# Performance work log

Hardware: AMD Instinct MI355X
Metric: run time of the kernel (lower is better)

The kernel has to match this reference:

```python
import jax, jax.numpy as jnp
import numpy as np

NUM_HEADS = 8
EMBED_DIM = 512
MAX_SEQ = 2048
HEAD_DIM = EMBED_DIM // NUM_HEADS
B, S = 2, 2048


def setup_inputs() -> dict:
    key = jax.random.key(0)
    ks = jax.random.split(key, 12)
    sd = 1.0 / np.sqrt(EMBED_DIM)
    return {
        "q_in": jax.random.normal(ks[0], (B, S, EMBED_DIM), jnp.float32),
        "k_in": jax.random.normal(ks[1], (B, S, EMBED_DIM), jnp.float32),
        "v_in": jax.random.normal(ks[2], (B, S, EMBED_DIM), jnp.float32),
        "Wq": jax.random.normal(ks[3], (EMBED_DIM, EMBED_DIM), jnp.float32) * sd,
        "bq": jnp.zeros((EMBED_DIM,), jnp.float32),
        "Wk": jax.random.normal(ks[4], (EMBED_DIM, EMBED_DIM), jnp.float32) * sd,
        "bk": jnp.zeros((EMBED_DIM,), jnp.float32),
        "Wv": jax.random.normal(ks[5], (EMBED_DIM, EMBED_DIM), jnp.float32) * sd,
        "bv": jnp.zeros((EMBED_DIM,), jnp.float32),
        "Wo": jax.random.normal(ks[6], (EMBED_DIM, EMBED_DIM), jnp.float32) * sd,
        "bo": jnp.zeros((EMBED_DIM,), jnp.float32),
        "rel_emb": jax.random.normal(ks[7], (MAX_SEQ, HEAD_DIM), jnp.float32) * sd,
    }


def _split_heads(x, W, b):
    # x: [B,S,E] -> [B,H,S,D]
    y = x @ W + b
    b_, s_ = y.shape[0], y.shape[1]
    return y.reshape(b_, s_, NUM_HEADS, HEAD_DIM).transpose(0, 2, 1, 3)


def _relative_scores(q, rel_emb):
    # q: [B,H,L,D]; rel_emb sliced to last L rows: [M,D] with M == L here
    L = q.shape[2]
    rel = rel_emb[max(0, MAX_SEQ - L):, :]
    M = rel.shape[0]
    scores = jnp.einsum('bhld,md->bhlm', q, rel)
    # mask = flip(tri(L,M), axis=-1): zero out future relative positions
    mask = jnp.flip(jnp.tri(L, M, dtype=jnp.float32), axis=1)
    scores = scores * mask
    # skew trick: pad one column on the left, reshape swapping last two dims, drop first row
    padded = jnp.pad(scores, ((0, 0), (0, 0), (0, 0), (1, 0)))  # [B,H,L,M+1]
    reshaped = padded.reshape(padded.shape[0], padded.shape[1], M + 1, L)
    skewed = reshaped[:, :, 1:, :]  # [B,H,M,L] == [B,H,L,L]
    return skewed


def reference(q_in, k_in, v_in, Wq, bq, Wk, bk, Wv, bv, Wo, bo, rel_emb):
    q = _split_heads(q_in, Wq, bq)  # [B,H,S,D]
    k = _split_heads(k_in, Wk, bk)
    v = _split_heads(v_in, Wv, bv)
    scores = jnp.einsum('bhqd,bhkd->bhqk', q, k)
    rel_scores = _relative_scores(q, rel_emb)
    logits = (scores + rel_scores) / jnp.sqrt(jnp.float32(HEAD_DIM))
    attn = jax.nn.softmax(logits, axis=-1)
    out = jnp.einsum('bhqk,bhkd->bhqd', attn, v)  # [B,H,S,D]
    merged = out.transpose(0, 2, 1, 3).reshape(out.shape[0], -1, EMBED_DIM)
    return merged @ Wo + bo, attn
```

## Files before the change

kernel.cpp:

```cpp
#include <hip/hip_runtime.h>


typedef __attribute__((ext_vector_type(4))) float f32x4;
typedef __attribute__((ext_vector_type(8))) short short8;

__device__ inline unsigned short f2bf(float x) {
    unsigned u = __float_as_uint(x);
    unsigned r = (u + 0x7fffu + ((u >> 16) & 1u)) >> 16;
    return (unsigned short)r;
}
__device__ inline float bf2f(unsigned short h) {
    return __uint_as_float(((unsigned)h) << 16);
}
__device__ inline int swz(int row, int bytecol) {
    return (row << 7) + (bytecol ^ ((row & 7) << 4));
}
__device__ inline void cvt4(float4 v, uint2& hi, uint2& lo) {
    unsigned short h0 = f2bf(v.x), h1 = f2bf(v.y), h2 = f2bf(v.z), h3 = f2bf(v.w);
    hi = make_uint2(((unsigned)h1 << 16) | h0, ((unsigned)h3 << 16) | h2);
    lo = make_uint2(((unsigned)f2bf(v.y - bf2f(h1)) << 16) | f2bf(v.x - bf2f(h0)),
                    ((unsigned)f2bf(v.w - bf2f(h3)) << 16) | f2bf(v.z - bf2f(h2)));
}

__global__ __launch_bounds__(256) void wt_prep4(const float* __restrict__ W0,
                                                const float* __restrict__ W1,
                                                const float* __restrict__ W2,
                                                const float* __restrict__ W3,
                                                unsigned short* __restrict__ wt)
{
    __shared__ float Ls[32][33];
    const int t = threadIdx.x;
    const int z = blockIdx.z;
    const float* W = (z == 0) ? W0 : (z == 1) ? W1 : (z == 2) ? W2 : W3;
    unsigned short* WTh = wt + (size_t)(2 * z) * 262144;
    unsigned short* WTl = wt + (size_t)(2 * z + 1) * 262144;
    const int k0 = blockIdx.x << 5, n0 = blockIdx.y << 5;
#pragma unroll
    for (int i = 0; i < 4; ++i) {
        int idx = (i << 8) + t;
        int kk = idx >> 5, nn = idx & 31;
        Ls[kk][nn] = W[(size_t)(k0 + kk) * 512 + n0 + nn];
    }
    __syncthreads();
#pragma unroll
    for (int i = 0; i < 2; ++i) {
        int idx = (i << 8) + t;
        int nn = idx >> 4, kp = idx & 15;
        float f0 = Ls[2 * kp][nn], f1 = Ls[2 * kp + 1][nn];
        unsigned short h0 = f2bf(f0), h1 = f2bf(f1);
        size_t off = (size_t)(n0 + nn) * 512 + k0 + 2 * kp;
        *(unsigned*)&WTh[off] = ((unsigned)h1 << 16) | h0;
        *(unsigned*)&WTl[off] = ((unsigned)f2bf(f1 - bf2f(h1)) << 16) | f2bf(f0 - bf2f(h0));
    }
}

__global__ __launch_bounds__(256) void rel_prep(const float* __restrict__ rel,
                                                unsigned short* __restrict__ relh)
{
    int idx = (blockIdx.x * 256 + threadIdx.x) << 3;
    float4 a = *(const float4*)&rel[idx];
    float4 b = *(const float4*)&rel[idx + 4];
    uint4 o;
    o.x = ((unsigned)f2bf(a.y) << 16) | f2bf(a.x);
    o.y = ((unsigned)f2bf(a.w) << 16) | f2bf(a.z);
    o.z = ((unsigned)f2bf(b.y) << 16) | f2bf(b.x);
    o.w = ((unsigned)f2bf(b.w) << 16) | f2bf(b.z);
    *(uint4*)&relh[idx] = o;
}

__device__ __forceinline__ void gemm64_core(const float* __restrict__ A,
                                            const unsigned short* __restrict__ WTh,
                                            const unsigned short* __restrict__ WTl,
                                            int m0, int n0, char* smem, int t,
                                            f32x4 (&acc)[4])
{
    char* aH = smem;
    char* aL = smem + 8192;
    char* wH = smem + 16384;
    char* wL = smem + 24576;
    const int lane = t & 63, w = t >> 6;
    const int lr = lane & 15, kg = lane >> 4;

    for (int k0 = 0; k0 < 512; k0 += 64) {
        if (k0) __syncthreads();
#pragma unroll
        for (int i = 0; i < 4; ++i) {
            int idx = (i << 8) + t;
            int row = idx >> 4, c4 = idx & 15;
            float4 v = *(const float4*)&A[(size_t)(m0 + row) * 512 + k0 + (c4 << 2)];
            uint2 hi, lo; cvt4(v, hi, lo);
            int ph = swz(row, c4 << 3);
            *(uint2*)(aH + ph) = hi;
            *(uint2*)(aL + ph) = lo;
        }
#pragma unroll
        for (int i = 0; i < 4; ++i) {
            int idx = (i << 8) + t;
            int plane = idx >> 9, rem = idx & 511;
            int nn = rem >> 3, j8 = rem & 7;
            const unsigned short* src = plane ? WTl : WTh;
            uint4 vv = *(const uint4*)&src[(size_t)(n0 + nn) * 512 + k0 + (j8 << 3)];
            *(uint4*)((plane ? wL : wH) + swz(nn, j8 << 4)) = vv;
        }
        __syncthreads();
#pragma unroll
        for (int kk = 0; kk < 2; ++kk) {
            int bc = (kk << 6) + (kg << 4);
            int ar = (w << 4) + lr;
            short8 a_h = *(const short8*)(aH + swz(ar, bc));
            short8 a_l = *(const short8*)(aL + swz(ar, bc));
#pragma unroll
            for (int f = 0; f < 4; ++f) {
                short8 b_h = *(const short8*)(wH + swz((f << 4) + lr, bc));
                short8 b_l = *(const short8*)(wL + swz((f << 4) + lr, bc));
                acc[f] = __builtin_amdgcn_mfma_f32_16x16x32_bf16(a_h, b_h, acc[f], 0, 0, 0);
                acc[f] = __builtin_amdgcn_mfma_f32_16x16x32_bf16(a_l, b_h, acc[f], 0, 0, 0);
                acc[f] = __builtin_amdgcn_mfma_f32_16x16x32_bf16(a_h, b_l, acc[f], 0, 0, 0);
            }
        }
    }
}

__global__ __launch_bounds__(256) void gemm_qkv(
    const float* __restrict__ Aq, const float* __restrict__ Ak, const float* __restrict__ Av,
    const unsigned short* __restrict__ wt,
    const float* __restrict__ bq, const float* __restrict__ bk, const float* __restrict__ bv,
    unsigned short* __restrict__ qh, unsigned short* __restrict__ ql,
    unsigned short* __restrict__ kh, unsigned short* __restrict__ kl,
    unsigned short* __restrict__ vh, unsigned short* __restrict__ vl)
{
    __shared__ char smem[32768];
    const int t = threadIdx.x;
    const int z = blockIdx.z;
    const int n0 = blockIdx.x << 6;
    const int m0 = blockIdx.y << 6;
    const int lane = t & 63, w = t >> 6;
    const int lr = lane & 15, kg = lane >> 4;

    const float* A = (z == 0) ? Aq : (z == 1) ? Ak : Av;
    const float* bias = (z == 0) ? bq : (z == 1) ? bk : bv;
    const unsigned short* WTh = wt + (size_t)(2 * z) * 262144;
    const unsigned short* WTl = wt + (size_t)(2 * z + 1) * 262144;
    unsigned short* outH = (z == 0) ? qh : (z == 1) ? kh : vh;
    unsigned short* outL = (z == 0) ? ql : (z == 1) ? kl : vl;

    f32x4 acc[4];
#pragma unroll
    for (int f = 0; f < 4; ++f) acc[f] = {0.f, 0.f, 0.f, 0.f};

    gemm64_core(A, WTh, WTl, m0, n0, smem, t, acc);

    const int mbase = m0 + (w << 4) + (kg << 2);
    const int b = mbase >> 11, s = mbase & 2047;
    const int bidx = (b << 3) + (n0 >> 6);
#pragma unroll
    for (int f = 0; f < 4; ++f) {
        int d = (f << 4) + lr;
        float bv_ = bias[n0 + d];
        if (z < 2) {
#pragma unroll
            for (int e = 0; e < 4; ++e) {
                float val = acc[f][e] + bv_;
                unsigned short hh = f2bf(val);
                size_t off = ((size_t)bidx * 2048 + s + e) * 64 + d;
                outH[off] = hh;
                outL[off] = f2bf(val - bf2f(hh));
            }
        } else {
            unsigned short h[4], l[4];
#pragma unroll
            for (int e = 0; e < 4; ++e) {
                float val = acc[f][e] + bv_;
                h[e] = f2bf(val);
                l[e] = f2bf(val - bf2f(h[e]));
            }
            size_t off = ((size_t)bidx * 64 + d) * 2048 + s;
            *(uint2*)&outH[off] = make_uint2(((unsigned)h[1] << 16) | h[0],
                                             ((unsigned)h[3] << 16) | h[2]);
            *(uint2*)&outL[off] = make_uint2(((unsigned)l[1] << 16) | l[0],
                                             ((unsigned)l[3] << 16) | l[2]);
        }
    }
}

__global__ __launch_bounds__(256) void gemm_out(
    const unsigned short* __restrict__ mWh, const unsigned short* __restrict__ mWl,
    const unsigned short* __restrict__ WTh, const unsigned short* __restrict__ WTl,
    const float* __restrict__ bias, float* __restrict__ out0)
{
    __shared__ char smem[32768];
    char* aH = smem;
    char* aL = smem + 8192;
    char* wH = smem + 16384;
    char* wL = smem + 24576;
    const int t = threadIdx.x;
    const int n0 = blockIdx.x << 6;
    const int m0 = blockIdx.y << 6;
    const int lane = t & 63, w = t >> 6;
    const int lr = lane & 15, kg = lane >> 4;

    f32x4 acc[4];
#pragma unroll
    for (int f = 0; f < 4; ++f) acc[f] = {0.f, 0.f, 0.f, 0.f};

    for (int k0 = 0; k0 < 512; k0 += 64) {
        if (k0) __syncthreads();
#pragma unroll
        for (int i = 0; i < 4; ++i) {
            int idx = (i << 8) + t;
            int plane = idx >> 9, rem = idx & 511;
            int row = rem >> 3, j8 = rem & 7;
            const unsigned short* src = plane ? mWl : mWh;
            uint4 vv = *(const uint4*)&src[(size_t)(m0 + row) * 512 + k0 + (j8 << 3)];
            *(uint4*)((plane ? aL : aH) + swz(row, j8 << 4)) = vv;
        }
#pragma unroll
        for (int i = 0; i < 4; ++i) {
            int idx = (i << 8) + t;
            int plane = idx >> 9, rem = idx & 511;
            int nn = rem >> 3, j8 = rem & 7;
            const unsigned short* src = plane ? WTl : WTh;
            uint4 vv = *(const uint4*)&src[(size_t)(n0 + nn) * 512 + k0 + (j8 << 3)];
            *(uint4*)((plane ? wL : wH) + swz(nn, j8 << 4)) = vv;
        }
        __syncthreads();
#pragma unroll
        for (int kk = 0; kk < 2; ++kk) {
            int bc = (kk << 6) + (kg << 4);
            int ar = (w << 4) + lr;
            short8 a_h = *(const short8*)(aH + swz(ar, bc));
            short8 a_l = *(const short8*)(aL + swz(ar, bc));
#pragma unroll
            for (int f = 0; f < 4; ++f) {
                short8 b_h = *(const short8*)(wH + swz((f << 4) + lr, bc));
                short8 b_l = *(const short8*)(wL + swz((f << 4) + lr, bc));
                acc[f] = __builtin_amdgcn_mfma_f32_16x16x32_bf16(a_h, b_h, acc[f], 0, 0, 0);
                acc[f] = __builtin_amdgcn_mfma_f32_16x16x32_bf16(a_l, b_h, acc[f], 0, 0, 0);
                acc[f] = __builtin_amdgcn_mfma_f32_16x16x32_bf16(a_h, b_l, acc[f], 0, 0, 0);
            }
        }
    }

    const int mbase = m0 + (w << 4) + (kg << 2);
#pragma unroll
    for (int f = 0; f < 4; ++f) {
        int n = n0 + (f << 4) + lr;
        float bv = bias[n];
#pragma unroll
        for (int e = 0; e < 4; ++e)
            out0[(size_t)(mbase + e) * 512 + n] = acc[f][e] + bv;
    }
}

__global__ __launch_bounds__(512, 4) void logits_flash(
    const unsigned short* __restrict__ qh_g, const unsigned short* __restrict__ ql_g,
    const unsigned short* __restrict__ kh_g, const unsigned short* __restrict__ kl_g,
    const unsigned short* __restrict__ relh_g,
    float* __restrict__ attn, float2* __restrict__ stats)
{
    __shared__ char smem[59136];
    char* kh = smem;
    char* kl = smem + 16384;
    char* bandP = smem + 32768;
    unsigned short* Pt = (unsigned short*)(smem + 32768);
    float* part_m = (float*)(smem + 58112);
    float* part_z = (float*)(smem + 58624);

    const int t = threadIdx.x;
    const int bh = blockIdx.y;
    int ib = blockIdx.x; if (bh & 8) ib = 31 - ib;
    const int i0 = ib << 6;
    const int lane = t & 63, w = t >> 6;
    const int wr = w >> 1, wc = w & 1;
    const int lr = lane & 15, kg = lane >> 4;
    const int irow = (wr << 4) + lr;

    const size_t qoff = ((size_t)bh * 2048 + i0 + irow) * 64;
    const short8 aH0 = *(const short8*)(qh_g + qoff + (kg << 3));
    const short8 aH1 = *(const short8*)(qh_g + qoff + 32 + (kg << 3));
    const short8 aL0 = *(const short8*)(ql_g + qoff + (kg << 3));
    const short8 aL1 = *(const short8*)(ql_g + qoff + 32 + (kg << 3));

    float rm = -3.0e38f, rz = 0.f;

    const unsigned short* khb = kh_g + (size_t)bh * 2048 * 64;
    const unsigned short* klb = kl_g + (size_t)bh * 2048 * 64;
    const size_t obase = ((size_t)bh * 2048 + i0) * 2048;

    for (int jt = 0; jt < 16; ++jt) {
        const int j0 = jt << 7;
        const bool anyRel = (j0 <= i0 + 63);
        const int m0 = 1984 - i0 + j0;
        __syncthreads();
        {
            int rr = t >> 2, gp = (t & 3) << 1;
            const unsigned short* s0 = khb + (size_t)(j0 + rr) * 64 + (gp << 3);
            *(uint4*)(kh + swz(rr, gp << 4)) = *(const uint4*)s0;
            *(uint4*)(kh + swz(rr, (gp + 1) << 4)) = *(const uint4*)(s0 + 8);
            const unsigned short* s1 = klb + (size_t)(j0 + rr) * 64 + (gp << 3);
            *(uint4*)(kl + swz(rr, gp << 4)) = *(const uint4*)s1;
            *(uint4*)(kl + swz(rr, (gp + 1) << 4)) = *(const uint4*)(s1 + 8);
        }
        if (anyRel) {
#pragma unroll
            for (int i = 0; i < 3; ++i) {
                int idx = (i << 9) + t;
                int row = idx >> 3, g = idx & 7;
                int m = m0 + row; if (m > 2047) m = 2047;
                *(uint4*)(bandP + swz(row, g << 4)) = *(const uint4*)(relh_g + (size_t)m * 64 + (g << 3));
            }
        }
        __syncthreads();

        f32x4 acc[4];
#pragma unroll
        for (int cf = 0; cf < 4; ++cf) {
            int krow = (wc << 6) + (cf << 4) + lr;
            short8 bH0 = *(const short8*)(kh + swz(krow, kg << 4));
            short8 bH1 = *(const short8*)(kh + swz(krow, 64 + (kg << 4)));
            short8 bL0 = *(const short8*)(kl + swz(krow, kg << 4));
            short8 bL1 = *(const short8*)(kl + swz(krow, 64 + (kg << 4)));
            f32x4 c = {0.f, 0.f, 0.f, 0.f};
            c = __builtin_amdgcn_mfma_f32_16x16x32_bf16(bH0, aH0, c, 0, 0, 0);
            c = __builtin_amdgcn_mfma_f32_16x16x32_bf16(bH1, aH1, c, 0, 0, 0);
            c = __builtin_amdgcn_mfma_f32_16x16x32_bf16(bH0, aL0, c, 0, 0, 0);
            c = __builtin_amdgcn_mfma_f32_16x16x32_bf16(bH1, aL1, c, 0, 0, 0);
            c = __builtin_amdgcn_mfma_f32_16x16x32_bf16(bL0, aH0, c, 0, 0, 0);
            c = __builtin_amdgcn_mfma_f32_16x16x32_bf16(bL1, aH1, c, 0, 0, 0);
            acc[cf] = c;
        }
        if (anyRel) {
            f32x4 pr[6];
#pragma unroll
            for (int q = 0; q < 6; ++q) {
                int ff = (wc ? 6 : 0) + q;
                int brow = (ff << 4) + lr;
                short8 rb0 = *(const short8*)(bandP + swz(brow, kg << 4));
                short8 rb1 = *(const short8*)(bandP + swz(brow, 64 + (kg << 4)));
                f32x4 c = {0.f, 0.f, 0.f, 0.f};
                c = __builtin_amdgcn_mfma_f32_16x16x32_bf16(rb0, aH0, c, 0, 0, 0);
                c = __builtin_amdgcn_mfma_f32_16x16x32_bf16(rb1, aH1, c, 0, 0, 0);
                pr[q] = c;
            }
            __syncthreads();
#pragma unroll
            for (int q = 0; q < 6; ++q) {
                int ff = (wc ? 6 : 0) + q;
#pragma unroll
                for (int e = 0; e < 4; ++e)
                    Pt[((ff << 4) + (kg << 2) + e) * 66 + irow] = f2bf(pr[q][e]);
            }
            __syncthreads();
        }

        float rowmax = -3.0e38f;
#pragma unroll
        for (int cf = 0; cf < 4; ++cf) {
            int jl0 = (wc << 6) + (cf << 4) + (kg << 2);
            f32x4 a = acc[cf];
#pragma unroll
            for (int e = 0; e < 4; ++e) {
                int jl = jl0 + e;
                if (anyRel && (jl - irow) <= (i0 - j0))
                    a[e] += bf2f(Pt[(jl + 63 - irow) * 66 + irow]);
            }
            acc[cf] = a;
            *(float4*)&attn[obase + (size_t)irow * 2048 + j0 + jl0] =
                make_float4(a[0], a[1], a[2], a[3]);
            rowmax = fmaxf(rowmax, fmaxf(fmaxf(a[0], a[1]), fmaxf(a[2], a[3])));
        }
        rowmax = fmaxf(rowmax, __shfl_xor(rowmax, 16, 64));
        rowmax = fmaxf(rowmax, __shfl_xor(rowmax, 32, 64));
        float zs = 0.f;
#pragma unroll
        for (int cf = 0; cf < 4; ++cf)
#pragma unroll
            for (int e = 0; e < 4; ++e)
                zs += __expf((acc[cf][e] - rowmax) * 0.125f);
        zs += __shfl_xor(zs, 16, 64);
        zs += __shfl_xor(zs, 32, 64);
        if (lane < 16) {
            part_m[(wc << 6) + irow] = rowmax;
            part_z[(wc << 6) + irow] = zs;
        }
        __syncthreads();
        if (t < 64) {
            float m1 = part_m[t], m2 = part_m[64 + t];
            float z1 = part_z[t], z2 = part_z[64 + t];
            float tm = fmaxf(m1, m2);
            float tz = z1 * __expf((m1 - tm) * 0.125f) + z2 * __expf((m2 - tm) * 0.125f);
            float mn = fmaxf(rm, tm);
            rz = rz * __expf((rm - mn) * 0.125f) + tz * __expf((tm - mn) * 0.125f);
            rm = mn;
        }
    }
    if (t < 64) stats[bh * 2048 + i0 + t] = make_float2(rm, 1.0f / rz);
}

__global__ __launch_bounds__(256) void pv_fused(float* __restrict__ attn,
                                                const unsigned short* __restrict__ vTh,
                                                const unsigned short* __restrict__ vTl,
                                                const float2* __restrict__ stats,
                                                float* __restrict__ pO)
{
    __shared__ char smem[33280];
    char* pH = smem;
    char* pL = smem + 8192;
    char* vH = smem + 16384;
    char* vL = smem + 24576;
    float2* sm = (float2*)(smem + 32768);

    const int t = threadIdx.x;
    const int i0 = blockIdx.x << 6;
    const int bh = blockIdx.y;
    const int jc = blockIdx.z;
    const int jc0 = jc << 10;
    const int lane = t & 63, w = t >> 6;
    const int lr = lane & 15, kg = lane >> 4;

    float* ab = attn + ((size_t)bh * 2048 + i0) * 2048;
    const unsigned short* vhb = vTh + (size_t)bh * 64 * 2048;
    const unsigned short* vlb = vTl + (size_t)bh * 64 * 2048;

    if (t < 64) sm[t] = stats[bh * 2048 + i0 + t];
    __syncthreads();

    f32x4 acc[4];
#pragma unroll
    for (int f = 0; f < 4; ++f) acc[f] = {0.f, 0.f, 0.f, 0.f};

    for (int j0 = jc0; j0 < jc0 + 1024; j0 += 64) {
        if (j0 != jc0) __syncthreads();
#pragma unroll
        for (int i = 0; i < 4; ++i) {
            int idx = (i << 8) + t;
            int row = idx >> 4, c4 = idx & 15;
            size_t go = (size_t)row * 2048 + j0 + (c4 << 2);
            float4 x = *(const float4*)&ab[go];
            float2 s2 = sm[row];
            float4 p;
            p.x = __expf((x.x - s2.x) * 0.125f) * s2.y;
            p.y = __expf((x.y - s2.x) * 0.125f) * s2.y;
            p.z = __expf((x.z - s2.x) * 0.125f) * s2.y;
            p.w = __expf((x.w - s2.x) * 0.125f) * s2.y;
            *(float4*)&ab[go] = p;
            uint2 hi, lo; cvt4(p, hi, lo);
            int ph = swz(row, c4 << 3);
            *(uint2*)(pH + ph) = hi;
            *(uint2*)(pL + ph) = lo;
        }
#pragma unroll
        for (int i = 0; i < 4; ++i) {
            int idx = (i << 8) + t;
            int plane = idx >> 9, rem = idx & 511;
            int d = rem >> 3, g8 = rem & 7;
            const unsigned short* src = (plane ? vlb : vhb) + (size_t)d * 2048 + j0 + (g8 << 3);
            *(uint4*)((plane ? vL : vH) + swz(d, g8 << 4)) = *(const uint4*)src;
        }
        __syncthreads();
#pragma unroll
        for (int kk = 0; kk < 2; ++kk) {
            int bc = (kk << 6) + (kg << 4);
            int ar = (w << 4) + lr;
            short8 a_h = *(const short8*)(pH + swz(ar, bc));
            short8 a_l = *(const short8*)(pL + swz(ar, bc));
#pragma unroll
            for (int f = 0; f < 4; ++f) {
                short8 b_h = *(const short8*)(vH + swz((f << 4) + lr, bc));
                short8 b_l = *(const short8*)(vL + swz((f << 4) + lr, bc));
                acc[f] = __builtin_amdgcn_mfma_f32_16x16x32_bf16(a_h, b_h, acc[f], 0, 0, 0);
                acc[f] = __builtin_amdgcn_mfma_f32_16x16x32_bf16(a_l, b_h, acc[f], 0, 0, 0);
                acc[f] = __builtin_amdgcn_mfma_f32_16x16x32_bf16(a_h, b_l, acc[f], 0, 0, 0);
            }
        }
    }
#pragma unroll
    for (int f = 0; f < 4; ++f) {
#pragma unroll
        for (int e = 0; e < 4; ++e) {
            int m = i0 + (w << 4) + (kg << 2) + e;
            pO[(size_t)jc * 2097152 + ((size_t)bh * 2048 + m) * 64 + (f << 4) + lr] = acc[f][e];
        }
    }
}

__global__ __launch_bounds__(256) void reduce_o(const float* __restrict__ pO,
                                                unsigned short* __restrict__ mWh,
                                                unsigned short* __restrict__ mWl)
{
    int fl = (blockIdx.x * 256 + threadIdx.x) << 2;
    float4 a = *(const float4*)&pO[fl];
    float4 b = *(const float4*)&pO[fl + 2097152];
    int bh = fl >> 17, rem = fl & 131071;
    int s = rem >> 6, d = rem & 63;
    float4 o = make_float4(a.x + b.x, a.y + b.y, a.z + b.z, a.w + b.w);
    uint2 hi, lo; cvt4(o, hi, lo);
    size_t off = (size_t)(((bh >> 3) << 11) + s) * 512 + ((bh & 7) << 6) + d;
    *(uint2*)&mWh[off] = hi;
    *(uint2*)&mWl[off] = lo;
}

extern "C" void kernel_launch(void* const* d_in, const int* in_sizes, int n_in,
                              void* d_out, int out_size, void* d_ws, size_t ws_size,
                              hipStream_t stream)
{
    const float* q_in = (const float*)d_in[0];
    const float* k_in = (const float*)d_in[1];
    const float* v_in = (const float*)d_in[2];
    const float* Wq   = (const float*)d_in[3];
    const float* bq   = (const float*)d_in[4];
    const float* Wk   = (const float*)d_in[5];
    const float* bk   = (const float*)d_in[6];
    const float* Wv   = (const float*)d_in[7];
    const float* bv   = (const float*)d_in[8];
    const float* Wo   = (const float*)d_in[9];
    const float* bo   = (const float*)d_in[10];
    const float* rel  = (const float*)d_in[11];

    float* out0 = (float*)d_out;
    float* attn = out0 + 2097152;

    float* ws = (float*)d_ws;
    unsigned short* qh = (unsigned short*)ws;
    unsigned short* ql = qh + 2097152;
    unsigned short* kh = (unsigned short*)(ws + 2097152);
    unsigned short* kl = kh + 2097152;
    unsigned short* vTh = (unsigned short*)(ws + 4194304);
    unsigned short* vTl = vTh + 2097152;
    unsigned short* wt = (unsigned short*)(ws + 6291456);
    unsigned short* relh = (unsigned short*)(ws + 7340032);
    float2* stats = (float2*)(ws + 7405568);
    float* pO = ws;
    unsigned short* mWh = (unsigned short*)(ws + 4194304);
    unsigned short* mWl = mWh + 2097152;

    wt_prep4<<<dim3(16, 16, 4), 256, 0, stream>>>(Wq, Wk, Wv, Wo, wt);
    rel_prep<<<64, 256, 0, stream>>>(rel, relh);

    gemm_qkv<<<dim3(8, 64, 3), 256, 0, stream>>>(q_in, k_in, v_in, wt,
                                                 bq, bk, bv,
                                                 qh, ql, kh, kl, vTh, vTl);

    logits_flash<<<dim3(32, 16), 512, 0, stream>>>(qh, ql, kh, kl, relh, attn, stats);
    pv_fused<<<dim3(32, 16, 2), 256, 0, stream>>>(attn, vTh, vTl, stats, pO);
    reduce_o<<<2048, 256, 0, stream>>>(pO, mWh, mWl);

    gemm_out<<<dim3(8, 64), 256, 0, stream>>>(mWh, mWl,
                                              wt + 6 * 262144, wt + 7 * 262144,
                                              bo, out0);
}
```

Baseline: 353.3 us.

## Remove LDS staging in pv_fused, load P and V fragments directly to registers

The PV kernel no longer stages normalized probabilities and V tiles through shared memory with barriers. Each lane now reads its own attention row segment, normalizes and writes it back, packs it into bf16 hi/lo MFMA operands in registers, and loads V fragments straight from global memory. This removes LDS traffic and __syncthreads, but the global accesses become less coalesced (row-strided 32-byte chunks per lane) and V is re-read by every wave instead of shared within the block.

```diff
diff --git a/kernel.cpp b/kernel.cpp
--- a/kernel.cpp
+++ b/kernel.cpp
@@ -20,6 +20,15 @@
     hi = make_uint2(((unsigned)h1 << 16) | h0, ((unsigned)h3 << 16) | h2);
     lo = make_uint2(((unsigned)f2bf(v.y - bf2f(h1)) << 16) | f2bf(v.x - bf2f(h0)),
                     ((unsigned)f2bf(v.w - bf2f(h3)) << 16) | f2bf(v.z - bf2f(h2)));
+}
+__device__ inline void pack8(float4 a, float4 b, short8& h8, short8& l8) {
+    float v[8] = {a.x, a.y, a.z, a.w, b.x, b.y, b.z, b.w};
+#pragma unroll
+    for (int i = 0; i < 8; ++i) {
+        unsigned short h = f2bf(v[i]);
+        h8[i] = (short)h;
+        l8[i] = (short)f2bf(v[i] - bf2f(h));
+    }
 }
 
 __global__ __launch_bounds__(256) void wt_prep4(const float* __restrict__ W0,
@@ -403,13 +412,6 @@
                                                 const float2* __restrict__ stats,
                                                 float* __restrict__ pO)
 {
-    __shared__ char smem[33280];
-    char* pH = smem;
-    char* pL = smem + 8192;
-    char* vH = smem + 16384;
-    char* vL = smem + 24576;
-    float2* sm = (float2*)(smem + 32768);
-
     const int t = threadIdx.x;
     const int i0 = blockIdx.x << 6;
     const int bh = blockIdx.y;
@@ -417,61 +419,50 @@
     const int jc0 = jc << 10;
     const int lane = t & 63, w = t >> 6;
     const int lr = lane & 15, kg = lane >> 4;
-
-    float* ab = attn + ((size_t)bh * 2048 + i0) * 2048;
+    const int irow = (w << 4) + lr;
+
+    float* arow = attn + ((size_t)bh * 2048 + i0 + irow) * 2048;
     const unsigned short* vhb = vTh + (size_t)bh * 64 * 2048;
     const unsigned short* vlb = vTl + (size_t)bh * 64 * 2048;
 
-    if (t < 64) sm[t] = stats[bh * 2048 + i0 + t];
-    __syncthreads();
+    const float2 s2 = stats[bh * 2048 + i0 + irow];
 
     f32x4 acc[4];
 #pragma unroll
     for (int f = 0; f < 4; ++f) acc[f] = {0.f, 0.f, 0.f, 0.f};
 
     for (int j0 = jc0; j0 < jc0 + 1024; j0 += 64) {
-        if (j0 != jc0) __syncthreads();
-#pragma unroll
-        for (int i = 0; i < 4; ++i) {
-            int idx = (i << 8) + t;
-            int row = idx >> 4, c4 = idx & 15;
-            size_t go = (size_t)row * 2048 + j0 + (c4 << 2);
-            float4 x = *(const float4*)&ab[go];
-            float2 s2 = sm[row];
-            float4 p;
-            p.x = __expf((x.x - s2.x) * 0.125f) * s2.y;
-            p.y = __expf((x.y - s2.x) * 0.125f) * s2.y;
-            p.z = __expf((x.z - s2.x) * 0.125f) * s2.y;
-            p.w = __expf((x.w - s2.x) * 0.125f) * s2.y;
-            *(float4*)&ab[go] = p;
-            uint2 hi, lo; cvt4(p, hi, lo);
-            int ph = swz(row, c4 << 3);
-            *(uint2*)(pH + ph) = hi;
-            *(uint2*)(pL + ph) = lo;
-        }
-#pragma unroll
-        for (int i = 0; i < 4; ++i) {
-            int idx = (i << 8) + t;
-            int plane = idx >> 9, rem = idx & 511;
-            int d = rem >> 3, g8 = rem & 7;
-            const unsigned short* src = (plane ? vlb : vhb) + (size_t)d * 2048 + j0 + (g8 << 3);
-            *(uint4*)((plane ? vL : vH) + swz(d, g8 << 4)) = *(const uint4*)src;
-        }
-        __syncthreads();
-#pragma unroll
-        for (int kk = 0; kk < 2; ++kk) {
-            int bc = (kk << 6) + (kg << 4);
-            int ar = (w << 4) + lr;
-            short8 a_h = *(const short8*)(pH + swz(ar, bc));
-            short8 a_l = *(const short8*)(pL + swz(ar, bc));
-#pragma unroll
-            for (int f = 0; f < 4; ++f) {
-                short8 b_h = *(const short8*)(vH + swz((f << 4) + lr, bc));
-                short8 b_l = *(const short8*)(vL + swz((f << 4) + lr, bc));
-                acc[f] = __builtin_amdgcn_mfma_f32_16x16x32_bf16(a_h, b_h, acc[f], 0, 0, 0);
-                acc[f] = __builtin_amdgcn_mfma_f32_16x16x32_bf16(a_l, b_h, acc[f], 0, 0, 0);
-                acc[f] = __builtin_amdgcn_mfma_f32_16x16x32_bf16(a_h, b_l, acc[f], 0, 0, 0);
-            }
+        const int c0 = j0 + (kg << 3);
+        float4 x0 = *(const float4*)&arow[c0];
+        float4 x1 = *(const float4*)&arow[c0 + 4];
+        float4 x2 = *(const float4*)&arow[c0 + 32];
+        float4 x3 = *(const float4*)&arow[c0 + 36];
+#define NRM(v) v.x = __expf((v.x - s2.x) * 0.125f) * s2.y; \
+               v.y = __expf((v.y - s2.x) * 0.125f) * s2.y; \
+               v.z = __expf((v.z - s2.x) * 0.125f) * s2.y; \
+               v.w = __expf((v.w - s2.x) * 0.125f) * s2.y;
+        NRM(x0) NRM(x1) NRM(x2) NRM(x3)
+#undef NRM
+        *(float4*)&arow[c0]      = x0;
+        *(float4*)&arow[c0 + 4]  = x1;
+        *(float4*)&arow[c0 + 32] = x2;
+        *(float4*)&arow[c0 + 36] = x3;
+        short8 ah0, al0, ah1, al1;
+        pack8(x0, x1, ah0, al0);
+        pack8(x2, x3, ah1, al1);
+#pragma unroll
+        for (int f = 0; f < 4; ++f) {
+            size_t vbase = (size_t)((f << 4) + lr) * 2048 + j0 + (kg << 3);
+            short8 bh0 = *(const short8*)(vhb + vbase);
+            short8 bl0 = *(const short8*)(vlb + vbase);
+            short8 bh1 = *(const short8*)(vhb + vbase + 32);
+            short8 bl1 = *(const short8*)(vlb + vbase + 32);
+            acc[f] = __builtin_amdgcn_mfma_f32_16x16x32_bf16(ah0, bh0, acc[f], 0, 0, 0);
+            acc[f] = __builtin_amdgcn_mfma_f32_16x16x32_bf16(al0, bh0, acc[f], 0, 0, 0);
+            acc[f] = __builtin_amdgcn_mfma_f32_16x16x32_bf16(ah0, bl0, acc[f], 0, 0, 0);
+            acc[f] = __builtin_amdgcn_mfma_f32_16x16x32_bf16(ah1, bh1, acc[f], 0, 0, 0);
+            acc[f] = __builtin_amdgcn_mfma_f32_16x16x32_bf16(al1, bh1, acc[f], 0, 0, 0);
+            acc[f] = __builtin_amdgcn_mfma_f32_16x16x32_bf16(ah1, bl1, acc[f], 0, 0, 0);
         }
     }
 #pragma unroll
```

Result: slower. 442.7 us (+25.3%).

## Fuse partial-output reduction into output GEMM and defer softmax stat merge

Applied to the files above, without the earlier changes.

The separate reduce_o kernel is removed. gemm_out now reads the two fp32 partial outputs directly, sums them, splits them into bf16 hi/lo pairs and stores those into shared memory. This drops one launch and an intermediate round trip through global memory, but each of the 8 column blocks now re-reads and re-converts the same A tile. In logits_flash, the per-tile merge of the row max and sum statistics moves to after the next iteration's barrier, which removes one __syncthreads per tile at the cost of a final merge after the loop.

```diff
diff --git a/kernel.cpp b/kernel.cpp
--- a/kernel.cpp
+++ b/kernel.cpp
@@ -184,7 +184,7 @@
 }
 
 __global__ __launch_bounds__(256) void gemm_out(
-    const unsigned short* __restrict__ mWh, const unsigned short* __restrict__ mWl,
+    const float* __restrict__ pO,
     const unsigned short* __restrict__ WTh, const unsigned short* __restrict__ WTl,
     const float* __restrict__ bias, float* __restrict__ out0)
 {
@@ -198,6 +198,7 @@
     const int m0 = blockIdx.y << 6;
     const int lane = t & 63, w = t >> 6;
     const int lr = lane & 15, kg = lane >> 4;
+    const int bq = m0 >> 11, s0 = m0 & 2047;
 
     f32x4 acc[4];
 #pragma unroll
@@ -205,14 +206,24 @@
 
     for (int k0 = 0; k0 < 512; k0 += 64) {
         if (k0) __syncthreads();
-#pragma unroll
-        for (int i = 0; i < 4; ++i) {
+        const float* p0 = pO + ((size_t)((bq << 3) + (k0 >> 6)) * 2048 + s0) * 64;
+#pragma unroll
+        for (int i = 0; i < 2; ++i) {
             int idx = (i << 8) + t;
-            int plane = idx >> 9, rem = idx & 511;
-            int row = rem >> 3, j8 = rem & 7;
-            const unsigned short* src = plane ? mWl : mWh;
-            uint4 vv = *(const uint4*)&src[(size_t)(m0 + row) * 512 + k0 + (j8 << 3)];
-            *(uint4*)((plane ? aL : aH) + swz(row, j8 << 4)) = vv;
+            int row = idx >> 3, j8 = idx & 7;
+            size_t off = (size_t)row * 64 + (j8 << 3);
+            float4 a0 = *(const float4*)&p0[off];
+            float4 a1 = *(const float4*)&p0[off + 4];
+            float4 b0 = *(const float4*)&p0[off + 2097152];
+            float4 b1 = *(const float4*)&p0[off + 4 + 2097152];
+            float4 v0 = make_float4(a0.x + b0.x, a0.y + b0.y, a0.z + b0.z, a0.w + b0.w);
+            float4 v1 = make_float4(a1.x + b1.x, a1.y + b1.y, a1.z + b1.z, a1.w + b1.w);
+            uint2 h0, l0, h1, l1;
+            cvt4(v0, h0, l0);
+            cvt4(v1, h1, l1);
+            int ph = swz(row, j8 << 4);
+            *(uint4*)(aH + ph) = make_uint4(h0.x, h0.y, h1.x, h1.y);
+            *(uint4*)(aL + ph) = make_uint4(l0.x, l0.y, l1.x, l1.y);
         }
 #pragma unroll
         for (int i = 0; i < 4; ++i) {
@@ -292,6 +303,15 @@
         const bool anyRel = (j0 <= i0 + 63);
         const int m0 = 1984 - i0 + j0;
         __syncthreads();
+        if (jt > 0 && t < 64) {
+            float m1 = part_m[t], m2 = part_m[64 + t];
+            float z1 = part_z[t], z2 = part_z[64 + t];
+            float tm = fmaxf(m1, m2);
+            float tz = z1 * __expf((m1 - tm) * 0.125f) + z2 * __expf((m2 - tm) * 0.125f);
+            float mn = fmaxf(rm, tm);
+            rz = rz * __expf((rm - mn) * 0.125f) + tz * __expf((tm - mn) * 0.125f);
+            rm = mn;
+        }
         {
             int rr = t >> 2, gp = (t & 3) << 1;
             const unsigned short* s0 = khb + (size_t)(j0 + rr) * 64 + (gp << 3);
@@ -383,18 +403,18 @@
             part_m[(wc << 6) + irow] = rowmax;
             part_z[(wc << 6) + irow] = zs;
         }
-        __syncthreads();
-        if (t < 64) {
-            float m1 = part_m[t], m2 = part_m[64 + t];
-            float z1 = part_z[t], z2 = part_z[64 + t];
-            float tm = fmaxf(m1, m2);
-            float tz = z1 * __expf((m1 - tm) * 0.125f) + z2 * __expf((m2 - tm) * 0.125f);
-            float mn = fmaxf(rm, tm);
-            rz = rz * __expf((rm - mn) * 0.125f) + tz * __expf((tm - mn) * 0.125f);
-            rm = mn;
-        }
-    }
-    if (t < 64) stats[bh * 2048 + i0 + t] = make_float2(rm, 1.0f / rz);
+    }
+    __syncthreads();
+    if (t < 64) {
+        float m1 = part_m[t], m2 = part_m[64 + t];
+        float z1 = part_z[t], z2 = part_z[64 + t];
+        float tm = fmaxf(m1, m2);
+        float tz = z1 * __expf((m1 - tm) * 0.125f) + z2 * __expf((m2 - tm) * 0.125f);
+        float mn = fmaxf(rm, tm);
+        rz = rz * __expf((rm - mn) * 0.125f) + tz * __expf((tm - mn) * 0.125f);
+        rm = mn;
+        stats[bh * 2048 + i0 + t] = make_float2(rm, 1.0f / rz);
+    }
 }
 
 __global__ __launch_bounds__(256) void pv_fused(float* __restrict__ attn,
@@ -484,22 +504,6 @@
     }
 }
 
-__global__ __launch_bounds__(256) void reduce_o(const float* __restrict__ pO,
-                                                unsigned short* __restrict__ mWh,
-                                                unsigned short* __restrict__ mWl)
-{
-    int fl = (blockIdx.x * 256 + threadIdx.x) << 2;
-    float4 a = *(const float4*)&pO[fl];
-    float4 b = *(const float4*)&pO[fl + 2097152];
-    int bh = fl >> 17, rem = fl & 131071;
-    int s = rem >> 6, d = rem & 63;
-    float4 o = make_float4(a.x + b.x, a.y + b.y, a.z + b.z, a.w + b.w);
-    uint2 hi, lo; cvt4(o, hi, lo);
-    size_t off = (size_t)(((bh >> 3) << 11) + s) * 512 + ((bh & 7) << 6) + d;
-    *(uint2*)&mWh[off] = hi;
-    *(uint2*)&mWl[off] = lo;
-}
-
 extern "C" void kernel_launch(void* const* d_in, const int* in_sizes, int n_in,
                               void* d_out, int out_size, void* d_ws, size_t ws_size,
                               hipStream_t stream)
@@ -531,8 +535,6 @@
     unsigned short* relh = (unsigned short*)(ws + 7340032);
     float2* stats = (float2*)(ws + 7405568);
     float* pO = ws;
-    unsigned short* mWh = (unsigned short*)(ws + 4194304);
-    unsigned short* mWl = mWh + 2097152;
 
     wt_prep4<<<dim3(16, 16, 4), 256, 0, stream>>>(Wq, Wk, Wv, Wo, wt);
     rel_prep<<<64, 256, 0, stream>>>(rel, relh);
@@ -543,9 +545,8 @@
 
     logits_flash<<<dim3(32, 16), 512, 0, stream>>>(qh, ql, kh, kl, relh, attn, stats);
     pv_fused<<<dim3(32, 16, 2), 256, 0, stream>>>(attn, vTh, vTl, stats, pO);
-    reduce_o<<<2048, 256, 0, stream>>>(pO, mWh, mWl);
-
-    gemm_out<<<dim3(8, 64), 256, 0, stream>>>(mWh, mWl,
+
+    gemm_out<<<dim3(8, 64), 256, 0, stream>>>(pO,
                                               wt + 6 * 262144, wt + 7 * 262144,
                                               bo, out0);
 }
```

New measurement: 348.6 us. About the same (-1.3%).
